# Performance work log

Measured on AMD Instinct MI355X. Metric: run time of the kernel, lower is better.

Reference implementation:

```python
import jax, jax.numpy as jnp
import numpy as np

C = 1.0            # PoincareBall curvature
BALL_EPS = 4e-3    # geoopt projx eps for float32
MIN_NORM = 1e-15


def artanh(x):
    x = jnp.clip(x, -1.0 + 1e-7, 1.0 - 1e-7)
    return 0.5 * (jnp.log1p(x) - jnp.log1p(-x))


def project(x):
    # geoopt projx: clip norm to (1 - eps) / sqrt(c)
    norm = jnp.maximum(jnp.linalg.norm(x, axis=-1, keepdims=True), MIN_NORM)
    maxnorm = (1.0 - BALL_EPS) / jnp.sqrt(C)
    return jnp.where(norm > maxnorm, x / norm * maxnorm, x)


def mobius_matvec(M, x):
    # geoopt mobius_matvec on PoincareBall (followed by project)
    sqrt_c = jnp.sqrt(C)
    x_norm = jnp.maximum(jnp.linalg.norm(x, axis=-1, keepdims=True), MIN_NORM)
    mx = x @ M.T
    mx_norm = jnp.maximum(jnp.linalg.norm(mx, axis=-1, keepdims=True), MIN_NORM)
    res = jnp.tanh(mx_norm / x_norm * artanh(sqrt_c * x_norm)) * mx / (mx_norm * sqrt_c)
    zero_mx = jnp.all(mx == 0.0, axis=-1, keepdims=True)
    return project(jnp.where(zero_mx, 0.0, res))


def mobius_add(x, y):
    # geoopt mobius_add on PoincareBall (followed by project)
    x2 = jnp.sum(x * x, axis=-1, keepdims=True)
    y2 = jnp.sum(y * y, axis=-1, keepdims=True)
    xy = jnp.sum(x * y, axis=-1, keepdims=True)
    num = (1.0 + 2.0 * C * xy + C * y2) * x + (1.0 - C * x2) * y
    den = jnp.maximum(1.0 + 2.0 * C * xy + C * C * x2 * y2, MIN_NORM)
    return project(num / den)


def hyp_linear(x, W, b):
    out = mobius_matvec(W, x)
    return mobius_add(out, b)


def hyperbolic_scores(q, k):
    # q, k: [B, H, S, Dh]
    eps = 1e-5
    q_norm_sq = jnp.minimum(jnp.sum(q * q, axis=-1, keepdims=True), 1.0 - eps)  # [B,H,S,1]
    k_norm_sq = jnp.minimum(jnp.sum(k * k, axis=-1, keepdims=True), 1.0 - eps)  # [B,H,S,1]
    qk = jnp.einsum('bhqd,bhkd->bhqk', q, k)
    k_norm_sq_t = jnp.swapaxes(k_norm_sq, -2, -1)                               # [B,H,1,S]
    denom = (1.0 - q_norm_sq) * (1.0 - k_norm_sq_t) + eps
    delta = 2.0 * ((qk - q_norm_sq * k_norm_sq_t) / denom)
    dist_sq = jnp.sqrt(jnp.maximum(delta, eps))
    return -dist_sq


def setup_inputs() -> dict:
    key = jax.random.key(0)
    B, S, E = 4, 2048, 512
    ks = jax.random.split(key, 5)
    x = jax.random.normal(ks[0], (B, S, E), dtype=jnp.float32) * 0.02  # inside unit ball
    bound = float(np.sqrt(6.0 / (E + E)))  # xavier_uniform
    def w(k):
        return jax.random.uniform(k, (E, E), dtype=jnp.float32, minval=-bound, maxval=bound)
    z = jnp.zeros((E,), dtype=jnp.float32)
    return {
        'x': x,
        'Wq': w(ks[1]), 'bq': z,
        'Wk': w(ks[2]), 'bk': z,
        'Wv': w(ks[3]), 'bv': z,
        'Wo': w(ks[4]), 'bo': z,
    }


def reference(x, Wq, bq, Wk, bk, Wv, bv, Wo, bo):
    B, S, E = x.shape
    H = 8
    Dh = E // H
    q = hyp_linear(x, Wq, bq)
    k = hyp_linear(x, Wk, bk)
    v = hyp_linear(x, Wv, bv)
    # [B,S,E] -> [B,H,S,Dh]
    split = lambda t: t.reshape(B, S, H, Dh).transpose(0, 2, 1, 3)
    q, k, v = split(q), split(k), split(v)
    scores = hyperbolic_scores(q, k) / jnp.sqrt(jnp.float32(Dh))
    attn = jax.nn.softmax(scores, axis=-1)
    out = jnp.einsum('bhqk,bhkd->bhqd', attn, v)
    out = out.transpose(0, 2, 1, 3).reshape(B, S, E)
    return hyp_linear(out, Wo, bo)
```

## Files before the change

kernel.cpp:

```cpp
#include <hip/hip_runtime.h>
#include <math.h>

#define B_ 4
#define S_ 2048
#define E_ 512
#define H_ 8
#define Dh_ 64
#define BS_ (B_*S_)
#define MAXN 0.996f

typedef __attribute__((ext_vector_type(8))) short short8;
typedef __attribute__((ext_vector_type(4))) float f32x4;

__device__ __forceinline__ unsigned f2bf(float x) {
  unsigned u = __float_as_uint(x);
  return (u + 0x7fffu + ((u >> 16) & 1u)) >> 16;
}
__device__ __forceinline__ float bf2f(unsigned b) {
  return __uint_as_float(b << 16);
}

__device__ __forceinline__ void gload_lds16(const void* g, void* lds) {
  __builtin_amdgcn_global_load_lds(
      (const __attribute__((address_space(1))) unsigned int*)g,
      (__attribute__((address_space(3))) unsigned int*)lds, 16, 0, 0);
}

__global__ __launch_bounds__(256) void pack_w_kernel(const float* __restrict__ W0,
    const float* __restrict__ W1, const float* __restrict__ W2,
    const float* __restrict__ W3, unsigned short* __restrict__ Wp) {
  const float* W = (blockIdx.y == 0) ? W0 : (blockIdx.y == 1) ? W1
                 : (blockIdx.y == 2) ? W2 : W3;
  unsigned short* dst = Wp + (size_t)blockIdx.y * 262144;
  int l = threadIdx.x & 63, tq = threadIdx.x >> 6;
  int n = blockIdx.x;
  int col = 16*n + (l & 15);
  int k0 = 8 * (l >> 4);
  #pragma unroll
  for (int tt = 0; tt < 4; ++tt) {
    int t = tq*4 + tt;
    const float* wp_ = W + (size_t)col * E_ + 32*t + k0;
    float4 a0 = *(const float4*)wp_, a1 = *(const float4*)(wp_ + 4);
    float av[8] = {a0.x,a0.y,a0.z,a0.w,a1.x,a1.y,a1.z,a1.w};
    short8 hi;
    #pragma unroll
    for (int j = 0; j < 8; ++j) hi[j] = (short)f2bf(av[j]);
    *(short8*)(dst + ((size_t)(t*32 + n))*512 + l*8) = hi;
  }
}

__global__ __launch_bounds__(256) void pack_x_kernel(const float* __restrict__ X,
    unsigned short* __restrict__ Xp, float* __restrict__ xn_out,
    float* __restrict__ art_out) {
  __shared__ float sm[4][16];
  int R16 = blockIdx.x;
  int tid = threadIdx.x;
  int wv = tid >> 6, l = tid & 63;
  int l15 = l & 15;
  const float* xrow = X + (size_t)(R16*16 + l15)*E_ + 8*(l >> 4);
  float xsq = 0.f;
  #pragma unroll
  for (int tt = 0; tt < 4; ++tt) {
    int t = wv*4 + tt;
    float4 c0 = *(const float4*)(xrow + 32*t);
    float4 c1 = *(const float4*)(xrow + 32*t + 4);
    float av[8] = {c0.x,c0.y,c0.z,c0.w,c1.x,c1.y,c1.z,c1.w};
    short8 hi, lo;
    #pragma unroll
    for (int j = 0; j < 8; ++j) {
      unsigned hb = f2bf(av[j]);
      hi[j] = (short)hb;
      lo[j] = (short)f2bf(av[j] - bf2f(hb));
      xsq = fmaf(av[j], av[j], xsq);
    }
    unsigned short* o = Xp + ((size_t)(R16*16 + t)*2)*512 + l*8;
    *(short8*)o = hi;
    *(short8*)(o + 512) = lo;
  }
  xsq += __shfl_xor(xsq, 16, 64);
  xsq += __shfl_xor(xsq, 32, 64);
  if (l < 16) sm[wv][l] = xsq;
  __syncthreads();
  if (tid < 16) {
    float s = sm[0][tid] + sm[1][tid] + sm[2][tid] + sm[3][tid];
    float xnv = fmaxf(sqrtf(s), 1e-15f);
    float aa = fminf(xnv, 1.f - 1e-7f);
    xn_out[R16*16 + tid] = xnv;
    art_out[R16*16 + tid] = 0.5f * (log1pf(aa) - log1pf(-aa));
  }
}

__global__ __launch_bounds__(256, 3) void qkv_linear(
    const unsigned short* __restrict__ Xp, const unsigned short* __restrict__ Wp,
    const float* __restrict__ bq_, const float* __restrict__ bk_,
    const float* __restrict__ bv_,
    unsigned short* __restrict__ Qhi, unsigned short* __restrict__ Khi,
    unsigned short* __restrict__ Vhi,
    const float* __restrict__ xn_arr, const float* __restrict__ art_arr,
    float* __restrict__ qn, float* __restrict__ kn, float* __restrict__ kni) {
  __shared__ float smM[2][4][4][4], smB[2][4][4][4], smb2[4];
  int tid = threadIdx.x;
  int w = tid >> 6, l = tid & 63;
  int l15 = l & 15, g = l >> 4;
  int R = blockIdx.x;
  int mat = blockIdx.y;
  const unsigned short* Wm = Wp + (size_t)mat * 262144;
  const float* bvec = (mat == 0) ? bq_ : (mat == 1) ? bk_ : bv_;
  unsigned short* outHi = (mat == 0) ? Qhi : (mat == 1) ? Khi : Vhi;
  float* normOut = (mat == 0) ? qn : kn;

  f32x4 acc0[8], acc1[8];
  #pragma unroll
  for (int s = 0; s < 8; ++s) {
    acc0[s] = (f32x4){0.f,0.f,0.f,0.f};
    acc1[s] = (f32x4){0.f,0.f,0.f,0.f};
  }
  const unsigned short* xp0 = Xp + ((size_t)(2*R)*16)*1024 + (size_t)l*8;
  const unsigned short* xp1 = Xp + ((size_t)(2*R+1)*16)*1024 + (size_t)l*8;
  const unsigned short* wl = Wm + (size_t)(8*w)*512 + (size_t)l*8;

  #pragma unroll 2
  for (int t = 0; t < 16; ++t) {
    const unsigned short* wb = wl + (size_t)t*16384;
    short8 b[8];
    #pragma unroll
    for (int s = 0; s < 8; ++s) b[s] = *(const short8*)(wb + s*512);
    short8 ahi0 = *(const short8*)(xp0 + t*1024);
    short8 alo0 = *(const short8*)(xp0 + t*1024 + 512);
    short8 ahi1 = *(const short8*)(xp1 + t*1024);
    short8 alo1 = *(const short8*)(xp1 + t*1024 + 512);
    #pragma unroll
    for (int s = 0; s < 8; ++s) {
      acc0[s] = __builtin_amdgcn_mfma_f32_16x16x32_bf16(ahi0, b[s], acc0[s], 0, 0, 0);
      acc0[s] = __builtin_amdgcn_mfma_f32_16x16x32_bf16(alo0, b[s], acc0[s], 0, 0, 0);
      acc1[s] = __builtin_amdgcn_mfma_f32_16x16x32_bf16(ahi1, b[s], acc1[s], 0, 0, 0);
      acc1[s] = __builtin_amdgcn_mfma_f32_16x16x32_bf16(alo1, b[s], acc1[s], 0, 0, 0);
    }
  }

  float xnv4[2][4], art4[2][4];
  #pragma unroll
  for (int rg = 0; rg < 2; ++rg)
    #pragma unroll
    for (int i = 0; i < 4; ++i) {
      int row = R*32 + rg*16 + 4*g + i;
      xnv4[rg][i] = xn_arr[row];
      art4[rg][i] = art_arr[row];
    }

  float bl[8];
  #pragma unroll
  for (int s = 0; s < 8; ++s) bl[s] = bvec[16*(8*w+s) + l15];
  float m2p[2][4] = {{0.f,0.f,0.f,0.f},{0.f,0.f,0.f,0.f}};
  float mbp[2][4] = {{0.f,0.f,0.f,0.f},{0.f,0.f,0.f,0.f}};
  float b2p = 0.f;
  #pragma unroll
  for (int s = 0; s < 8; ++s) {
    b2p += bl[s]*bl[s];
    #pragma unroll
    for (int i = 0; i < 4; ++i) {
      m2p[0][i] = fmaf(acc0[s][i], acc0[s][i], m2p[0][i]);
      mbp[0][i] = fmaf(acc0[s][i], bl[s], mbp[0][i]);
      m2p[1][i] = fmaf(acc1[s][i], acc1[s][i], m2p[1][i]);
      mbp[1][i] = fmaf(acc1[s][i], bl[s], mbp[1][i]);
    }
  }
  #pragma unroll
  for (int off = 1; off <= 8; off <<= 1) {
    b2p += __shfl_xor(b2p, off, 64);
    #pragma unroll
    for (int rg = 0; rg < 2; ++rg)
      #pragma unroll
      for (int i = 0; i < 4; ++i) {
        m2p[rg][i] += __shfl_xor(m2p[rg][i], off, 64);
        mbp[rg][i] += __shfl_xor(mbp[rg][i], off, 64);
      }
  }
  if (l == 0) smb2[w] = b2p;
  if (l15 == 0) {
    #pragma unroll
    for (int rg = 0; rg < 2; ++rg)
      #pragma unroll
      for (int i = 0; i < 4; ++i) { smM[rg][w][g][i] = m2p[rg][i]; smB[rg][w][g][i] = mbp[rg][i]; }
  }
  __syncthreads();
  float b2 = smb2[0] + smb2[1] + smb2[2] + smb2[3];
  float G[2][4], Hc[2][4];
  #pragma unroll
  for (int rg = 0; rg < 2; ++rg)
    #pragma unroll
    for (int i = 0; i < 4; ++i) {
      float m2 = smM[rg][0][g][i]+smM[rg][1][g][i]+smM[rg][2][g][i]+smM[rg][3][g][i];
      float mb = smB[rg][0][g][i]+smB[rg][1][g][i]+smB[rg][2][g][i]+smB[rg][3][g][i];
      float xn = xnv4[rg][i], art = art4[rg][i];
      float mn = fmaxf(sqrtf(m2), 1e-15f);
      float t = tanhf(mn / xn * art);
      float alpha, rn;
      if (m2 > 0.f) { alpha = t / mn; rn = t; } else { alpha = 0.f; rn = 0.f; }
      if (rn > MAXN) { alpha *= MAXN / rn; rn = MAXN; }
      float x2r = rn * rn;
      float xy = alpha * mb;
      float A  = 1.f + 2.f*xy + b2;
      float Bc = 1.f - x2r;
      float den = fmaxf(1.f + 2.f*xy + x2r*b2, 1e-15f);
      float n2v = (A*A*x2r + 2.f*A*Bc*xy + Bc*Bc*b2) / (den*den);
      float nn = fmaxf(sqrtf(n2v), 1e-15f);
      float sc = (nn > MAXN) ? (MAXN / nn) : 1.f;
      G[rg][i]  = sc * A * alpha / den;
      Hc[rg][i] = sc * Bc / den;
    }

  #pragma unroll
  for (int rg = 0; rg < 2; ++rg) {
    const f32x4* acc = rg ? acc1 : acc0;
    #pragma unroll
    for (int i = 0; i < 4; ++i) {
      int grow = R*32 + rg*16 + 4*g + i;
      int bb = grow >> 11, seq = grow & 2047;
      int tile = seq >> 6;
      float hn0 = 0.f, hn1 = 0.f;
      #pragma unroll
      for (int s = 0; s < 8; ++s) {
        int col = 16*(8*w+s) + l15;
        float v = G[rg][i]*acc[s][i] + Hc[rg][i]*bl[s];
        int h = col >> 6, c = col & 63;
        size_t base;
        if (mat == 2) {
          int kt = (seq >> 5) & 1, gp = (seq >> 3) & 3, jv = seq & 7;
          int dn = c >> 4, lt = (c & 15) | (gp << 4);
          base = ((size_t)((bb*8 + h)*32 + tile))*4096 + (size_t)((kt*4+dn)*64 + lt)*8 + jv;
        } else {
          int nf = (seq >> 4) & 3, lt15 = seq & 15;
          int dt = c >> 5, m = (c >> 3) & 3, j = c & 7;
          base = ((size_t)((bb*8 + h)*32 + tile))*4096 + (size_t)((dt*4+nf)*64 + (lt15|(m<<4)))*8 + j;
        }
        outHi[base] = (unsigned short)f2bf(v);
        if (mat < 2) { if (s < 4) hn0 += v*v; else hn1 += v*v; }
      }
      if (mat < 2) {
        hn0 += __shfl_xor(hn0,1,64); hn0 += __shfl_xor(hn0,2,64);
        hn0 += __shfl_xor(hn0,4,64); hn0 += __shfl_xor(hn0,8,64);
        hn1 += __shfl_xor(hn1,1,64); hn1 += __shfl_xor(hn1,2,64);
        hn1 += __shfl_xor(hn1,4,64); hn1 += __shfl_xor(hn1,8,64);
        if (l15 == 0) {
          float h0 = fminf(hn0, 1.f - 1e-5f), h1 = fminf(hn1, 1.f - 1e-5f);
          size_t i0 = ((size_t)(bb*8 + 2*w + 0))*S_ + seq;
          size_t i1 = ((size_t)(bb*8 + 2*w + 1))*S_ + seq;
          normOut[i0] = h0;
          normOut[i1] = h1;
          if (mat == 1) {
            kni[i0] = 1.f / sqrtf(1.f - h0);
            kni[i1] = 1.f / sqrtf(1.f - h1);
          }
        }
      }
    }
  }
}

__global__ __launch_bounds__(256, 3) void o_linear(const float* __restrict__ X,
    const unsigned short* __restrict__ Wp, const float* __restrict__ bvec,
    float* __restrict__ outF) {
  __shared__ float smM[2][4][4][4], smB[2][4][4][4], smb2[4];
  int tid = threadIdx.x;
  int w = tid >> 6, l = tid & 63;
  int l15 = l & 15, g = l >> 4;
  int R = blockIdx.x;

  f32x4 acc0[8], acc1[8];
  #pragma unroll
  for (int s = 0; s < 8; ++s) {
    acc0[s] = (f32x4){0.f,0.f,0.f,0.f};
    acc1[s] = (f32x4){0.f,0.f,0.f,0.f};
  }
  const float* xrow0 = X + (size_t)(R*32 + l15)*E_ + 8*g;
  const float* xrow1 = xrow0 + (size_t)16*E_;
  const unsigned short* wl = Wp + (size_t)(8*w)*512 + (size_t)l*8;

  float4 p00 = *(const float4*)xrow0, p01 = *(const float4*)(xrow0 + 4);
  float4 p10 = *(const float4*)xrow1, p11 = *(const float4*)(xrow1 + 4);
  float xsq0 = 0.f, xsq1 = 0.f;

  #pragma unroll 1
  for (int t = 0; t < 16; ++t) {
    const unsigned short* wb = wl + (size_t)t*16384;
    short8 b[8];
    #pragma unroll
    for (int s = 0; s < 8; ++s) b[s] = *(const short8*)(wb + s*512);
    float a0v[8] = {p00.x,p00.y,p00.z,p00.w,p01.x,p01.y,p01.z,p01.w};
    float a1v[8] = {p10.x,p10.y,p10.z,p10.w,p11.x,p11.y,p11.z,p11.w};
    short8 ahi0, alo0, ahi1, alo1;
    #pragma unroll
    for (int j = 0; j < 8; ++j) {
      unsigned hb0 = f2bf(a0v[j]);
      ahi0[j] = (short)hb0;
      alo0[j] = (short)f2bf(a0v[j] - bf2f(hb0));
      xsq0 = fmaf(a0v[j], a0v[j], xsq0);
      unsigned hb1 = f2bf(a1v[j]);
      ahi1[j] = (short)hb1;
      alo1[j] = (short)f2bf(a1v[j] - bf2f(hb1));
      xsq1 = fmaf(a1v[j], a1v[j], xsq1);
    }
    if (t < 15) {
      p00 = *(const float4*)(xrow0 + 32*(t+1));
      p01 = *(const float4*)(xrow0 + 32*(t+1) + 4);
      p10 = *(const float4*)(xrow1 + 32*(t+1));
      p11 = *(const float4*)(xrow1 + 32*(t+1) + 4);
    }
    #pragma unroll
    for (int s = 0; s < 8; ++s) {
      acc0[s] = __builtin_amdgcn_mfma_f32_16x16x32_bf16(ahi0, b[s], acc0[s], 0, 0, 0);
      acc0[s] = __builtin_amdgcn_mfma_f32_16x16x32_bf16(alo0, b[s], acc0[s], 0, 0, 0);
      acc1[s] = __builtin_amdgcn_mfma_f32_16x16x32_bf16(ahi1, b[s], acc1[s], 0, 0, 0);
      acc1[s] = __builtin_amdgcn_mfma_f32_16x16x32_bf16(alo1, b[s], acc1[s], 0, 0, 0);
    }
  }

  xsq0 += __shfl_xor(xsq0, 16, 64); xsq0 += __shfl_xor(xsq0, 32, 64);
  xsq1 += __shfl_xor(xsq1, 16, 64); xsq1 += __shfl_xor(xsq1, 32, 64);
  float xnv4[2][4], art4[2][4];
  #pragma unroll
  for (int i = 0; i < 4; ++i) {
    float s20 = __shfl(xsq0, 4*g + i, 64);
    float s21 = __shfl(xsq1, 4*g + i, 64);
    float xn0 = fmaxf(sqrtf(s20), 1e-15f);
    float xn1 = fmaxf(sqrtf(s21), 1e-15f);
    float aa0 = fminf(xn0, 1.f - 1e-7f);
    float aa1 = fminf(xn1, 1.f - 1e-7f);
    xnv4[0][i] = xn0; art4[0][i] = 0.5f * (log1pf(aa0) - log1pf(-aa0));
    xnv4[1][i] = xn1; art4[1][i] = 0.5f * (log1pf(aa1) - log1pf(-aa1));
  }

  float bl[8];
  #pragma unroll
  for (int s = 0; s < 8; ++s) bl[s] = bvec[16*(8*w+s) + l15];
  float m2p[2][4] = {{0.f,0.f,0.f,0.f},{0.f,0.f,0.f,0.f}};
  float mbp[2][4] = {{0.f,0.f,0.f,0.f},{0.f,0.f,0.f,0.f}};
  float b2p = 0.f;
  #pragma unroll
  for (int s = 0; s < 8; ++s) {
    b2p += bl[s]*bl[s];
    #pragma unroll
    for (int i = 0; i < 4; ++i) {
      m2p[0][i] = fmaf(acc0[s][i], acc0[s][i], m2p[0][i]);
      mbp[0][i] = fmaf(acc0[s][i], bl[s], mbp[0][i]);
      m2p[1][i] = fmaf(acc1[s][i], acc1[s][i], m2p[1][i]);
      mbp[1][i] = fmaf(acc1[s][i], bl[s], mbp[1][i]);
    }
  }
  #pragma unroll
  for (int off = 1; off <= 8; off <<= 1) {
    b2p += __shfl_xor(b2p, off, 64);
    #pragma unroll
    for (int rg = 0; rg < 2; ++rg)
      #pragma unroll
      for (int i = 0; i < 4; ++i) {
        m2p[rg][i] += __shfl_xor(m2p[rg][i], off, 64);
        mbp[rg][i] += __shfl_xor(mbp[rg][i], off, 64);
      }
  }
  if (l == 0) smb2[w] = b2p;
  if (l15 == 0) {
    #pragma unroll
    for (int rg = 0; rg < 2; ++rg)
      #pragma unroll
      for (int i = 0; i < 4; ++i) { smM[rg][w][g][i] = m2p[rg][i]; smB[rg][w][g][i] = mbp[rg][i]; }
  }
  __syncthreads();
  float b2 = smb2[0] + smb2[1] + smb2[2] + smb2[3];
  #pragma unroll
  for (int rg = 0; rg < 2; ++rg) {
    const f32x4* acc = rg ? acc1 : acc0;
    #pragma unroll
    for (int i = 0; i < 4; ++i) {
      float m2 = smM[rg][0][g][i]+smM[rg][1][g][i]+smM[rg][2][g][i]+smM[rg][3][g][i];
      float mb = smB[rg][0][g][i]+smB[rg][1][g][i]+smB[rg][2][g][i]+smB[rg][3][g][i];
      float xn = xnv4[rg][i], art = art4[rg][i];
      float mn = fmaxf(sqrtf(m2), 1e-15f);
      float t = tanhf(mn / xn * art);
      float alpha, rn;
      if (m2 > 0.f) { alpha = t / mn; rn = t; } else { alpha = 0.f; rn = 0.f; }
      if (rn > MAXN) { alpha *= MAXN / rn; rn = MAXN; }
      float x2r = rn * rn;
      float xy = alpha * mb;
      float A  = 1.f + 2.f*xy + b2;
      float Bc = 1.f - x2r;
      float den = fmaxf(1.f + 2.f*xy + x2r*b2, 1e-15f);
      float n2v = (A*A*x2r + 2.f*A*Bc*xy + Bc*Bc*b2) / (den*den);
      float nn = fmaxf(sqrtf(n2v), 1e-15f);
      float sc = (nn > MAXN) ? (MAXN / nn) : 1.f;
      float Gv = sc * A * alpha / den;
      float Hv = sc * Bc / den;
      int grow = R*32 + rg*16 + 4*g + i;
      #pragma unroll
      for (int s = 0; s < 8; ++s)
        outF[(size_t)grow*E_ + 16*(8*w+s) + l15] = Gv*acc[s][i] + Hv*bl[s];
    }
  }
}

__global__ __launch_bounds__(256, 4) void attn_kernel(
    const unsigned short* __restrict__ Qhi, const unsigned short* __restrict__ Khi,
    const unsigned short* __restrict__ Vhi,
    const float* __restrict__ qn_arr, const float* __restrict__ kn_arr,
    const float* __restrict__ kni_arr, float* __restrict__ Out) {
  __shared__ __align__(16) unsigned short Kf[2][4096];
  __shared__ __align__(16) unsigned short Vf[2][4096];
  __shared__ __align__(16) unsigned short Pf[4][1024];

  int tid = threadIdx.x;
  int w = tid >> 6, l = tid & 63;
  int l15 = l & 15, g = l >> 4;

  int bid = blockIdx.x;
  int xcd = bid & 7, idx = bid >> 3;
  int bh = xcd * 4 + (idx >> 5);
  int qblk = idx & 31;
  int b = bh >> 3, h = bh & 7;
  int qb = qblk * 64;

  const unsigned short* qbase = Qhi + ((size_t)(bh*32 + qblk))*4096;
  short8 qhi[2];
  #pragma unroll
  for (int dt = 0; dt < 2; ++dt)
    qhi[dt] = *(const short8*)(qbase + (size_t)((dt*4 + w)*64 + l)*8);
  float qnv[4], pr[4];
  #pragma unroll
  for (int i = 0; i < 4; ++i) {
    qnv[i] = qn_arr[(size_t)bh*S_ + qb + 16*w + 4*g + i];
    pr[i] = -0.25503386f * __builtin_amdgcn_rsqf(1.f - qnv[i]);
  }

  f32x4 Oacc[4];
  #pragma unroll
  for (int dn = 0; dn < 4; ++dn) Oacc[dn] = (f32x4){0.f,0.f,0.f,0.f};
  float lp[4] = {0.f,0.f,0.f,0.f};

  const unsigned short* Kbh = Khi + ((size_t)bh*32)*4096;
  const unsigned short* Vbh = Vhi + ((size_t)bh*32)*4096;
  const float* knp  = kn_arr  + (size_t)bh*S_;
  const float* knip = kni_arr + (size_t)bh*S_;

  #pragma unroll
  for (int r = 0; r < 2; ++r) {
    gload_lds16(Kbh + r*2048 + w*512 + l*8, &Kf[0][r*2048 + w*512]);
    gload_lds16(Vbh + r*2048 + w*512 + l*8, &Vf[0][r*2048 + w*512]);
  }
  asm volatile("s_waitcnt vmcnt(0)" ::: "memory");
  __syncthreads();

  #pragma unroll 1
  for (int tile = 0; tile < 32; ++tile) {
    int cur = tile & 1;
    int kb = tile * 64;
    float knc[4], kin[4];
    #pragma unroll
    for (int n = 0; n < 4; ++n) {
      knc[n] = knp[kb + 16*n + l15];
      kin[n] = knip[kb + 16*n + l15];
    }
    if (tile < 31) {
      const unsigned short* kp = Kbh + ((size_t)(tile+1))*4096;
      const unsigned short* vp = Vbh + ((size_t)(tile+1))*4096;
      #pragma unroll
      for (int r = 0; r < 2; ++r) {
        gload_lds16(kp + r*2048 + w*512 + l*8, &Kf[cur^1][r*2048 + w*512]);
        gload_lds16(vp + r*2048 + w*512 + l*8, &Vf[cur^1][r*2048 + w*512]);
      }
    }
    __builtin_amdgcn_sched_barrier(0);
    #pragma unroll
    for (int n = 0; n < 4; ++n) {
      f32x4 Cn = (f32x4){0.f,0.f,0.f,0.f};
      #pragma unroll
      for (int dt = 0; dt < 2; ++dt) {
        short8 kfr = *(const short8*)&Kf[cur][((dt*4 + n)*64 + l)*8];
        Cn = __builtin_amdgcn_mfma_f32_16x16x32_bf16(qhi[dt], kfr, Cn, 0, 0, 0);
      }
      int cbase = (n >> 1)*64 + 16*((2*n + (l15 >> 3)) & 3) + 4*g;
      int csb = cbase ^ ((cbase >> 3) & 7);
      int j7 = l15 & 7;
      #pragma unroll
      for (int i = 0; i < 4; ++i) {
        float num = fmaf(-qnv[i], knc[n], Cn[i]);
        float d2 = fmaxf(num, 5e-6f);
        float sq = d2 * __builtin_amdgcn_rsqf(d2);
        float p = __builtin_amdgcn_exp2f(pr[i] * kin[n] * sq);
        unsigned u = __float_as_uint(p);
        lp[i] += __uint_as_float(u & 0xffff0000u);
        Pf[w][((csb ^ i) << 3) + j7] = (unsigned short)(u >> 16);
      }
    }
    short8 pa0, pa1;
    { int c = l;       int cs = c ^ ((c >> 3) & 7); pa0 = *(const short8*)&Pf[w][cs*8]; }
    { int c = 64 + l;  int cs = c ^ ((c >> 3) & 7); pa1 = *(const short8*)&Pf[w][cs*8]; }
    #pragma unroll
    for (int dn = 0; dn < 4; ++dn) {
      short8 v0 = *(const short8*)&Vf[cur][((0*4 + dn)*64 + l)*8];
      short8 v1 = *(const short8*)&Vf[cur][((1*4 + dn)*64 + l)*8];
      f32x4 o = Oacc[dn];
      o = __builtin_amdgcn_mfma_f32_16x16x32_bf16(pa0, v0, o, 0, 0, 0);
      o = __builtin_amdgcn_mfma_f32_16x16x32_bf16(pa1, v1, o, 0, 0, 0);
      Oacc[dn] = o;
    }
    asm volatile("s_waitcnt vmcnt(0)" ::: "memory");
    __builtin_amdgcn_s_barrier();
  }

  #pragma unroll
  for (int i = 0; i < 4; ++i) {
    lp[i] += __shfl_xor(lp[i], 1, 64);
    lp[i] += __shfl_xor(lp[i], 2, 64);
    lp[i] += __shfl_xor(lp[i], 4, 64);
    lp[i] += __shfl_xor(lp[i], 8, 64);
    lp[i] = 1.f / lp[i];
  }
  #pragma unroll
  for (int i = 0; i < 4; ++i) {
    size_t orow = (size_t)(b*S_ + qb + 16*w + 4*g + i)*E_ + h*Dh_;
    #pragma unroll
    for (int dn = 0; dn < 4; ++dn)
      Out[orow + 16*dn + l15] = Oacc[dn][i] * lp[i];
  }
}

extern "C" void kernel_launch(void* const* d_in, const int* in_sizes, int n_in,
                              void* d_out, int out_size, void* d_ws, size_t ws_size,
                              hipStream_t stream) {
  const float* x  = (const float*)d_in[0];
  const float* Wq = (const float*)d_in[1];
  const float* bq = (const float*)d_in[2];
  const float* Wk = (const float*)d_in[3];
  const float* bk = (const float*)d_in[4];
  const float* Wv = (const float*)d_in[5];
  const float* bv = (const float*)d_in[6];
  const float* Wo = (const float*)d_in[7];
  const float* bo = (const float*)d_in[8];
  float* out = (float*)d_out;

  char* p = (char*)d_ws;
  unsigned short* Wp  = (unsigned short*)p; p += (size_t)2  << 20;
  unsigned short* Xp  = (unsigned short*)p; p += (size_t)17 << 20;
  unsigned short* Qhi = (unsigned short*)p; p += (size_t)8  << 20;
  unsigned short* Khi = (unsigned short*)p; p += (size_t)8  << 20;
  unsigned short* Vhi = (unsigned short*)p; p += (size_t)8  << 20;
  float* ao   = (float*)p; p += (size_t)16 << 20;
  float* xn   = (float*)p; p += BS_ * 4;
  float* art  = (float*)p; p += BS_ * 4;
  float* qn   = (float*)p; p += (size_t)B_*H_*S_ * 4;
  float* kn   = (float*)p; p += (size_t)B_*H_*S_ * 4;
  float* kni  = (float*)p; p += (size_t)B_*H_*S_ * 4;

  pack_w_kernel<<<dim3(32, 4), dim3(256), 0, stream>>>(Wq, Wk, Wv, Wo, Wp);
  pack_x_kernel<<<dim3(BS_/16), dim3(256), 0, stream>>>(x, Xp, xn, art);
  qkv_linear<<<dim3(BS_/32, 3), dim3(256), 0, stream>>>(Xp, Wp, bq, bk, bv,
                                                        Qhi, Khi, Vhi, xn, art, qn, kn, kni);
  attn_kernel<<<dim3(1024), dim3(256), 0, stream>>>(Qhi, Khi, Vhi, qn, kn, kni, ao);
  o_linear<<<dim3(BS_/32), dim3(256), 0, stream>>>(ao, Wp + 3*262144, bo, out);
}
```

Baseline: 146.0 us.

## Process two query row-groups per wave to reuse K/V tiles in attention

Each wave now handles 32 query rows (two 16-row groups) instead of 16, so every block covers 128 queries and the grid is halved to 512 blocks. Each K/V fragment read from LDS feeds two MFMAs, and each K/V tile loaded from global memory serves twice as many queries. This aims to cut LDS and global traffic per unit of work. The cost is roughly double the accumulator registers, a larger P buffer in shared memory, lower occupancy (launch bounds 2) and fewer blocks to spread across CUs.

```diff
diff --git a/kernel.cpp b/kernel.cpp
--- a/kernel.cpp
+++ b/kernel.cpp
@@ -399,14 +399,14 @@
   }
 }
 
-__global__ __launch_bounds__(256, 4) void attn_kernel(
+__global__ __launch_bounds__(256, 2) void attn_kernel(
     const unsigned short* __restrict__ Qhi, const unsigned short* __restrict__ Khi,
     const unsigned short* __restrict__ Vhi,
     const float* __restrict__ qn_arr, const float* __restrict__ kn_arr,
     const float* __restrict__ kni_arr, float* __restrict__ Out) {
   __shared__ __align__(16) unsigned short Kf[2][4096];
   __shared__ __align__(16) unsigned short Vf[2][4096];
-  __shared__ __align__(16) unsigned short Pf[4][1024];
+  __shared__ __align__(16) unsigned short Pf[4][2][1024];
 
   int tid = threadIdx.x;
   int w = tid >> 6, l = tid & 63;
@@ -414,27 +414,38 @@
 
   int bid = blockIdx.x;
   int xcd = bid & 7, idx = bid >> 3;
-  int bh = xcd * 4 + (idx >> 5);
-  int qblk = idx & 31;
+  int bh = xcd * 4 + (idx >> 4);
+  int qblk = idx & 15;
   int b = bh >> 3, h = bh & 7;
-  int qb = qblk * 64;
-
-  const unsigned short* qbase = Qhi + ((size_t)(bh*32 + qblk))*4096;
-  short8 qhi[2];
-  #pragma unroll
-  for (int dt = 0; dt < 2; ++dt)
-    qhi[dt] = *(const short8*)(qbase + (size_t)((dt*4 + w)*64 + l)*8);
-  float qnv[4], pr[4];
-  #pragma unroll
-  for (int i = 0; i < 4; ++i) {
-    qnv[i] = qn_arr[(size_t)bh*S_ + qb + 16*w + 4*g + i];
-    pr[i] = -0.25503386f * __builtin_amdgcn_rsqf(1.f - qnv[i]);
-  }
-
-  f32x4 Oacc[4];
-  #pragma unroll
-  for (int dn = 0; dn < 4; ++dn) Oacc[dn] = (f32x4){0.f,0.f,0.f,0.f};
-  float lp[4] = {0.f,0.f,0.f,0.f};
+  int qb = qblk * 128;
+
+  short8 qhi[2][2];
+  float qnv[2][4], pr[2][4];
+  #pragma unroll
+  for (int rg = 0; rg < 2; ++rg) {
+    int rw = 2*w + rg;
+    int qtile = qblk*2 + (rw >> 2);
+    int nf = rw & 3;
+    const unsigned short* qbase = Qhi + ((size_t)(bh*32 + qtile))*4096;
+    #pragma unroll
+    for (int dt = 0; dt < 2; ++dt)
+      qhi[rg][dt] = *(const short8*)(qbase + (size_t)((dt*4 + nf)*64 + l)*8);
+    #pragma unroll
+    for (int i = 0; i < 4; ++i) {
+      qnv[rg][i] = qn_arr[(size_t)bh*S_ + qb + rw*16 + 4*g + i];
+      pr[rg][i] = -0.25503386f * __builtin_amdgcn_rsqf(1.f - qnv[rg][i]);
+    }
+  }
+
+  f32x4 Oacc[2][4];
+  float lp[2][4];
+  #pragma unroll
+  for (int rg = 0; rg < 2; ++rg)
+    #pragma unroll
+    for (int dn = 0; dn < 4; ++dn) {
+      Oacc[rg][dn] = (f32x4){0.f,0.f,0.f,0.f};
+      lp[rg][dn] = 0.f;
+    }
 
   const unsigned short* Kbh = Khi + ((size_t)bh*32)*4096;
   const unsigned short* Vbh = Vhi + ((size_t)bh*32)*4096;
@@ -471,56 +482,74 @@
     __builtin_amdgcn_sched_barrier(0);
     #pragma unroll
     for (int n = 0; n < 4; ++n) {
-      f32x4 Cn = (f32x4){0.f,0.f,0.f,0.f};
+      f32x4 C0 = (f32x4){0.f,0.f,0.f,0.f};
+      f32x4 C1 = (f32x4){0.f,0.f,0.f,0.f};
       #pragma unroll
       for (int dt = 0; dt < 2; ++dt) {
         short8 kfr = *(const short8*)&Kf[cur][((dt*4 + n)*64 + l)*8];
-        Cn = __builtin_amdgcn_mfma_f32_16x16x32_bf16(qhi[dt], kfr, Cn, 0, 0, 0);
+        C0 = __builtin_amdgcn_mfma_f32_16x16x32_bf16(qhi[0][dt], kfr, C0, 0, 0, 0);
+        C1 = __builtin_amdgcn_mfma_f32_16x16x32_bf16(qhi[1][dt], kfr, C1, 0, 0, 0);
       }
       int cbase = (n >> 1)*64 + 16*((2*n + (l15 >> 3)) & 3) + 4*g;
       int csb = cbase ^ ((cbase >> 3) & 7);
       int j7 = l15 & 7;
       #pragma unroll
       for (int i = 0; i < 4; ++i) {
-        float num = fmaf(-qnv[i], knc[n], Cn[i]);
-        float d2 = fmaxf(num, 5e-6f);
-        float sq = d2 * __builtin_amdgcn_rsqf(d2);
-        float p = __builtin_amdgcn_exp2f(pr[i] * kin[n] * sq);
-        unsigned u = __float_as_uint(p);
-        lp[i] += __uint_as_float(u & 0xffff0000u);
-        Pf[w][((csb ^ i) << 3) + j7] = (unsigned short)(u >> 16);
-      }
-    }
-    short8 pa0, pa1;
-    { int c = l;       int cs = c ^ ((c >> 3) & 7); pa0 = *(const short8*)&Pf[w][cs*8]; }
-    { int c = 64 + l;  int cs = c ^ ((c >> 3) & 7); pa1 = *(const short8*)&Pf[w][cs*8]; }
+        float num0 = fmaf(-qnv[0][i], knc[n], C0[i]);
+        float d20 = fmaxf(num0, 5e-6f);
+        float sq0 = d20 * __builtin_amdgcn_rsqf(d20);
+        float p0 = __builtin_amdgcn_exp2f(pr[0][i] * kin[n] * sq0);
+        unsigned u0 = __float_as_uint(p0);
+        lp[0][i] += __uint_as_float(u0 & 0xffff0000u);
+        Pf[w][0][((csb ^ i) << 3) + j7] = (unsigned short)(u0 >> 16);
+        float num1 = fmaf(-qnv[1][i], knc[n], C1[i]);
+        float d21 = fmaxf(num1, 5e-6f);
+        float sq1 = d21 * __builtin_amdgcn_rsqf(d21);
+        float p1 = __builtin_amdgcn_exp2f(pr[1][i] * kin[n] * sq1);
+        unsigned u1 = __float_as_uint(p1);
+        lp[1][i] += __uint_as_float(u1 & 0xffff0000u);
+        Pf[w][1][((csb ^ i) << 3) + j7] = (unsigned short)(u1 >> 16);
+      }
+    }
+    short8 pa[2][2];
+    #pragma unroll
+    for (int rg = 0; rg < 2; ++rg) {
+      { int c = l;      int cs = c ^ ((c >> 3) & 7); pa[rg][0] = *(const short8*)&Pf[w][rg][cs*8]; }
+      { int c = 64 + l; int cs = c ^ ((c >> 3) & 7); pa[rg][1] = *(const short8*)&Pf[w][rg][cs*8]; }
+    }
     #pragma unroll
     for (int dn = 0; dn < 4; ++dn) {
       short8 v0 = *(const short8*)&Vf[cur][((0*4 + dn)*64 + l)*8];
       short8 v1 = *(const short8*)&Vf[cur][((1*4 + dn)*64 + l)*8];
-      f32x4 o = Oacc[dn];
-      o = __builtin_amdgcn_mfma_f32_16x16x32_bf16(pa0, v0, o, 0, 0, 0);
-      o = __builtin_amdgcn_mfma_f32_16x16x32_bf16(pa1, v1, o, 0, 0, 0);
-      Oacc[dn] = o;
+      #pragma unroll
+      for (int rg = 0; rg < 2; ++rg) {
+        f32x4 o = Oacc[rg][dn];
+        o = __builtin_amdgcn_mfma_f32_16x16x32_bf16(pa[rg][0], v0, o, 0, 0, 0);
+        o = __builtin_amdgcn_mfma_f32_16x16x32_bf16(pa[rg][1], v1, o, 0, 0, 0);
+        Oacc[rg][dn] = o;
+      }
     }
     asm volatile("s_waitcnt vmcnt(0)" ::: "memory");
     __builtin_amdgcn_s_barrier();
   }
 
   #pragma unroll
-  for (int i = 0; i < 4; ++i) {
-    lp[i] += __shfl_xor(lp[i], 1, 64);
-    lp[i] += __shfl_xor(lp[i], 2, 64);
-    lp[i] += __shfl_xor(lp[i], 4, 64);
-    lp[i] += __shfl_xor(lp[i], 8, 64);
-    lp[i] = 1.f / lp[i];
-  }
-  #pragma unroll
-  for (int i = 0; i < 4; ++i) {
-    size_t orow = (size_t)(b*S_ + qb + 16*w + 4*g + i)*E_ + h*Dh_;
-    #pragma unroll
-    for (int dn = 0; dn < 4; ++dn)
-      Out[orow + 16*dn + l15] = Oacc[dn][i] * lp[i];
+  for (int rg = 0; rg < 2; ++rg) {
+    #pragma unroll
+    for (int i = 0; i < 4; ++i) {
+      lp[rg][i] += __shfl_xor(lp[rg][i], 1, 64);
+      lp[rg][i] += __shfl_xor(lp[rg][i], 2, 64);
+      lp[rg][i] += __shfl_xor(lp[rg][i], 4, 64);
+      lp[rg][i] += __shfl_xor(lp[rg][i], 8, 64);
+      lp[rg][i] = 1.f / lp[rg][i];
+    }
+    #pragma unroll
+    for (int i = 0; i < 4; ++i) {
+      size_t orow = (size_t)(b*S_ + qb + (2*w+rg)*16 + 4*g + i)*E_ + h*Dh_;
+      #pragma unroll
+      for (int dn = 0; dn < 4; ++dn)
+        Out[orow + 16*dn + l15] = Oacc[rg][dn][i] * lp[rg][i];
+    }
   }
 }
 
@@ -555,6 +584,6 @@
   pack_x_kernel<<<dim3(BS_/16), dim3(256), 0, stream>>>(x, Xp, xn, art);
   qkv_linear<<<dim3(BS_/32, 3), dim3(256), 0, stream>>>(Xp, Wp, bq, bk, bv,
                                                         Qhi, Khi, Vhi, xn, art, qn, kn, kni);
-  attn_kernel<<<dim3(1024), dim3(256), 0, stream>>>(Qhi, Khi, Vhi, qn, kn, kni, ao);
+  attn_kernel<<<dim3(512), dim3(256), 0, stream>>>(Qhi, Khi, Vhi, qn, kn, kni, ao);
   o_linear<<<dim3(BS_/32), dim3(256), 0, stream>>>(ao, Wp + 3*262144, bo, out);
 }
```

After: 147.5 us. No clear change (+1.0%).
